# Performance work log

Measured on AMD Instinct MI355X. Metric: run time of the kernel, lower is better.

The kernel has to match this reference:

```python
import jax, jax.numpy as jnp
import numpy as np

N = 100_000   # nodes
D = 128       # emb_size
E = 1_600_000 # edges (avg degree 16)
K = 64        # K1 (channel 0 pooling clusters)
LAYERS = 2


def _l2norm(x):
    # F.normalize(x, dim=-1, p=2) with eps=1e-12
    return x / jnp.maximum(jnp.linalg.norm(x, axis=-1, keepdims=True), 1e-12)


def setup_inputs() -> dict:
    key = jax.random.key(0)
    ks = jax.random.split(key, 9)
    return {
        "adj": jax.random.uniform(ks[0], (N,), dtype=jnp.float32),
        "edge_row": jax.random.randint(ks[1], (E,), 0, N),
        "edge_col": jax.random.randint(ks[2], (E,), 0, N),
        "edge_val": jax.random.uniform(ks[3], (E,), dtype=jnp.float32),
        "embedding": jax.random.normal(ks[4], (N, D), dtype=jnp.float32) * 0.02,
        "W_item0": jax.random.normal(ks[5], (D, D), dtype=jnp.float32) * 0.05,
        "W_item1": jax.random.normal(ks[6], (D, D), dtype=jnp.float32) * 0.05,
        "W_i1": jax.random.normal(ks[7], (D, D), dtype=jnp.float32) * 0.05,
        "W_i2": jax.random.normal(ks[8], (D, K), dtype=jnp.float32) * 0.05,
        "channel": 0,
    }


def reference(adj, edge_row, edge_col, edge_val, embedding,
              W_item0, W_item1, W_i1, W_i2, channel):
    n = adj.shape[0]

    def spmm(x):  # sparse [N,N] @ dense [N,D] via COO gather + segment_sum
        return jax.ops.segment_sum(edge_val[:, None] * x[edge_col], edge_row,
                                   num_segments=n)

    x = embedding
    final = [x]
    finalh = []
    for W in (W_item0, W_item1):  # structurally distinct per-layer weights
        x = spmm(x @ W)                                   # [N,D]
        H1 = jax.nn.relu(x @ W_i1 + x)                    # [N,D]
        H1 = jax.nn.softmax(H1 @ W_i2, axis=1)            # [N,K]
        h = H1.T * adj                                    # [K,N]
        h = h * (1.0 / (jnp.sum(h, axis=0) + 1e-8))       # column-normalize
        h = H1 @ (h @ x)                                  # [N,K]@[K,D] -> [N,D]
        x = h + x
        final.append(_l2norm(x))
        finalh.append(_l2norm(h))
    item_embeddings = sum(final) / (LAYERS + 1)
    hs = sum(finalh) / LAYERS
    return item_embeddings, hs
```

## Files before the change

### kernel.cpp

```cpp
#include <hip/hip_runtime.h>

constexpr int DD = 128;
constexpr int KK = 64;
constexpr int NBLK_C2 = 512;
constexpr int CH = 512;

typedef __attribute__((ext_vector_type(8))) short bf16x8;
typedef __attribute__((ext_vector_type(4))) float f32x4;

union U4 { unsigned u[4]; int4 i4; bf16x8 v; };

__device__ inline unsigned bf16_rne(float x) {
  unsigned u = __float_as_uint(x);
  u += 0x7fff + ((u >> 16) & 1);
  return u >> 16;
}
__device__ inline float bf16f(unsigned h) { return __uint_as_float(h << 16); }
__device__ inline void split2(float a, float b, unsigned& hi, unsigned& lo) {
  const unsigned h0 = bf16_rne(a), h1 = bf16_rne(b);
  const unsigned l0 = bf16_rne(a - bf16f(h0)), l1 = bf16_rne(b - bf16f(h1));
  hi = h0 | (h1 << 16);
  lo = l0 | (l1 << 16);
}

__global__ void k_prepW(const float* __restrict__ W, unsigned* __restrict__ Whi,
                        unsigned* __restrict__ Wlo) {
  const int id = blockIdx.x * 256 + threadIdx.x;
  const int j = id & 3, l = (id >> 2) & 63, t = (id >> 8) & 7, ks = id >> 11;
  const int k0 = 32 * ks + 8 * (l >> 4) + 2 * j;
  const int col = 16 * t + (l & 15);
  const float e0 = W[k0 * 128 + col], e1 = W[(k0 + 1) * 128 + col];
  unsigned hi, lo;
  split2(e0, e1, hi, lo);
  Whi[id] = hi;
  Wlo[id] = lo;
}

__global__ void k_prepWs(const float* __restrict__ W, unsigned* __restrict__ Wf) {
  const int id = blockIdx.x * 256 + threadIdx.x;
  const int j = id & 3, l = (id >> 2) & 63, t = (id >> 8) & 3, ks = id >> 10;
  const int k0 = 32 * ks + 8 * (l >> 4) + 2 * j;
  const int col = 16 * t + (l & 15);
  const unsigned h0 = bf16_rne(W[k0 * 64 + col]);
  const unsigned h1 = bf16_rne(W[(k0 + 1) * 64 + col]);
  Wf[id] = h0 | (h1 << 16);
}

__global__ void k_prepM(const float* __restrict__ M, unsigned* __restrict__ Mhi,
                        unsigned* __restrict__ Mlo) {
  const int id = blockIdx.x * 256 + threadIdx.x;
  const int j = id & 3, l = (id >> 2) & 63, t = (id >> 8) & 7, ks = id >> 11;
  const int k0 = 32 * ks + 8 * (l >> 4) + 2 * j;
  const int col = 16 * t + (l & 15);
  unsigned hi, lo;
  split2(M[k0 * 128 + col], M[(k0 + 1) * 128 + col], hi, lo);
  Mhi[id] = hi;
  Mlo[id] = lo;
}

__global__ __launch_bounds__(512) void k_gemm_mfma(const float* __restrict__ X,
                                                   const unsigned* __restrict__ Whi,
                                                   const unsigned* __restrict__ Wlo,
                                                   unsigned short* __restrict__ Yb,
                                                   int n) {
  __shared__ unsigned sb[2 * 8192];
  {
    const int t = threadIdx.x;
    uint4* d0 = (uint4*)sb;
    const uint4* s0 = (const uint4*)Whi;
#pragma unroll
    for (int i = 0; i < 4; ++i) d0[t + 512 * i] = s0[t + 512 * i];
    uint4* d1 = (uint4*)(sb + 8192);
    const uint4* s1 = (const uint4*)Wlo;
#pragma unroll
    for (int i = 0; i < 4; ++i) d1[t + 512 * i] = s1[t + 512 * i];
  }
  __syncthreads();
  const int wave = threadIdx.x >> 6, lane = threadIdx.x & 63;
  const int l15 = lane & 15, lhi = lane >> 4;
  const int row0 = blockIdx.x * 256 + wave * 32;
  if (row0 >= n) return;
  f32x4 acc[2][8];
#pragma unroll
  for (int rt = 0; rt < 2; ++rt)
#pragma unroll
    for (int t = 0; t < 8; ++t) acc[rt][t] = (f32x4){0.f, 0.f, 0.f, 0.f};
#pragma unroll
  for (int ks = 0; ks < 4; ++ks) {
    U4 ah[2], al[2];
#pragma unroll
    for (int rt = 0; rt < 2; ++rt) {
      int r = row0 + rt * 16 + l15;
      if (r >= n) r = n - 1;
      const float4 x0 = *(const float4*)&X[(size_t)r * DD + ks * 32 + lhi * 8];
      const float4 x1 = *(const float4*)&X[(size_t)r * DD + ks * 32 + lhi * 8 + 4];
      split2(x0.x, x0.y, ah[rt].u[0], al[rt].u[0]);
      split2(x0.z, x0.w, ah[rt].u[1], al[rt].u[1]);
      split2(x1.x, x1.y, ah[rt].u[2], al[rt].u[2]);
      split2(x1.z, x1.w, ah[rt].u[3], al[rt].u[3]);
    }
#pragma unroll
    for (int t = 0; t < 8; ++t) {
      U4 bh, bl;
      const int off = ((ks * 8 + t) * 64 + lane) * 4;
      bh.i4 = *(const int4*)&sb[off];
      bl.i4 = *(const int4*)&sb[8192 + off];
#pragma unroll
      for (int rt = 0; rt < 2; ++rt) {
        acc[rt][t] = __builtin_amdgcn_mfma_f32_16x16x32_bf16(ah[rt].v, bh.v, acc[rt][t], 0, 0, 0);
        acc[rt][t] = __builtin_amdgcn_mfma_f32_16x16x32_bf16(al[rt].v, bh.v, acc[rt][t], 0, 0, 0);
        acc[rt][t] = __builtin_amdgcn_mfma_f32_16x16x32_bf16(ah[rt].v, bl.v, acc[rt][t], 0, 0, 0);
      }
    }
  }
#pragma unroll
  for (int rt = 0; rt < 2; ++rt)
#pragma unroll
    for (int rr = 0; rr < 4; ++rr) {
      const int row = row0 + rt * 16 + lhi * 4 + rr;
      if (row < n) {
#pragma unroll
        for (int t = 0; t < 8; ++t)
          Yb[(size_t)row * DD + t * 16 + l15] =
              (unsigned short)bf16_rne(acc[rt][t][rr]);
      }
    }
}

__global__ void k_hist(const int* __restrict__ er, int* __restrict__ cnt, int E) {
  for (long e = (long)blockIdx.x * blockDim.x + threadIdx.x; e < E;
       e += (long)gridDim.x * blockDim.x)
    atomicAdd(&cnt[er[e]], 1);
}

__global__ __launch_bounds__(256) void k_chunksum(const int* __restrict__ cnt,
                                                  int* __restrict__ csum, int n) {
  const int c = blockIdx.x, t = threadIdx.x;
  const int i0 = c * CH + 2 * t;
  int s2 = 0;
  if (i0 < n) s2 += cnt[i0];
  if (i0 + 1 < n) s2 += cnt[i0 + 1];
#pragma unroll
  for (int off = 32; off >= 1; off >>= 1) s2 += __shfl_xor(s2, off);
  __shared__ int ws_[4];
  if ((t & 63) == 0) ws_[t >> 6] = s2;
  __syncthreads();
  if (t == 0) csum[c] = ws_[0] + ws_[1] + ws_[2] + ws_[3];
}

__global__ __launch_bounds__(256) void k_chunkscan(const int* __restrict__ csum,
                                                   int* __restrict__ coff, int nch) {
  __shared__ int s[256];
  const int t = threadIdx.x;
  const int v = (t < nch) ? csum[t] : 0;
  s[t] = v;
  __syncthreads();
  for (int off = 1; off < 256; off <<= 1) {
    const int u = (t >= off) ? s[t - off] : 0;
    __syncthreads();
    s[t] += u;
    __syncthreads();
  }
  coff[t] = s[t] - v;
}

__global__ __launch_bounds__(256) void k_rowptr(const int* __restrict__ cnt,
                                                const int* __restrict__ coff,
                                                int* __restrict__ rowptr,
                                                int n, int E) {
  const int c = blockIdx.x, t = threadIdx.x;
  const int i0 = c * CH + 2 * t, i1 = i0 + 1;
  const int v0 = (i0 < n) ? cnt[i0] : 0;
  const int v1 = (i1 < n) ? cnt[i1] : 0;
  __shared__ int s[256];
  const int s2 = v0 + v1;
  s[t] = s2;
  __syncthreads();
  for (int off = 1; off < 256; off <<= 1) {
    const int u = (t >= off) ? s[t - off] : 0;
    __syncthreads();
    s[t] += u;
    __syncthreads();
  }
  const int excl = s[t] - s2 + coff[c];
  if (i0 < n) rowptr[i0] = excl;
  if (i1 < n) rowptr[i1] = excl + v0;
  if (c == 0 && t == 0) rowptr[n] = E;
}

__global__ void k_scatter(const int* __restrict__ er, const int* __restrict__ ec,
                          const float* __restrict__ ev,
                          const int* __restrict__ rowptr, int* __restrict__ cur,
                          int2* __restrict__ erec, int E, int n) {
  const int rng = blockIdx.x & 7;
  const int g = blockIdx.x >> 3;
  const long e_lo = (long)g * E / 256;
  const long e_hi = (long)(g + 1) * E / 256;
  const int r_lo = (int)((long)rng * n / 8);
  const int r_hi = (int)((long)(rng + 1) * n / 8);
  for (long e = e_lo + threadIdx.x; e < e_hi; e += 256) {
    const int r = er[e];
    if (r >= r_lo && r < r_hi) {
      const int pos = rowptr[r] + atomicAdd(&cur[r], 1);
      erec[pos] = make_int2(ec[e], __float_as_int(ev[e]));
    }
  }
}

__global__ __launch_bounds__(256) void k_spmm_csr(const int* __restrict__ rowptr,
                                                  const int2* __restrict__ erec,
                                                  const unsigned* __restrict__ Yb,
                                                  float* __restrict__ Xo, int n) {
  const int lane = threadIdx.x & 63;
  const int c0 = 2 * lane;
  const long gw = (long)blockIdx.x * 4 + (threadIdx.x >> 6);
  const long nw = (long)gridDim.x * 4;
  for (long row = gw; row < n; row += nw) {
    const int b = rowptr[row], e2 = rowptr[row + 1];
    float a0 = 0.f, a1 = 0.f, b0 = 0.f, b1 = 0.f;
    float c00 = 0.f, c1 = 0.f, d0 = 0.f, d1 = 0.f;
    int e = b;
    for (; e + 4 <= e2; e += 4) {
      const int2 r0 = erec[e], r1 = erec[e + 1];
      const int2 r2 = erec[e + 2], r3 = erec[e + 3];
      const unsigned q0 = Yb[(size_t)r0.x * (DD / 2) + lane];
      const unsigned q1 = Yb[(size_t)r1.x * (DD / 2) + lane];
      const unsigned q2 = Yb[(size_t)r2.x * (DD / 2) + lane];
      const unsigned q3 = Yb[(size_t)r3.x * (DD / 2) + lane];
      const float v0 = __int_as_float(r0.y), v1 = __int_as_float(r1.y);
      const float v2 = __int_as_float(r2.y), v3 = __int_as_float(r3.y);
      a0 = fmaf(v0, __uint_as_float(q0 << 16), a0);
      a1 = fmaf(v0, __uint_as_float(q0 & 0xffff0000u), a1);
      b0 = fmaf(v1, __uint_as_float(q1 << 16), b0);
      b1 = fmaf(v1, __uint_as_float(q1 & 0xffff0000u), b1);
      c00 = fmaf(v2, __uint_as_float(q2 << 16), c00);
      c1 = fmaf(v2, __uint_as_float(q2 & 0xffff0000u), c1);
      d0 = fmaf(v3, __uint_as_float(q3 << 16), d0);
      d1 = fmaf(v3, __uint_as_float(q3 & 0xffff0000u), d1);
    }
    for (; e + 2 <= e2; e += 2) {
      const int2 r0 = erec[e], r1 = erec[e + 1];
      const float v0 = __int_as_float(r0.y), v1 = __int_as_float(r1.y);
      const unsigned q0 = Yb[(size_t)r0.x * (DD / 2) + lane];
      const unsigned q1 = Yb[(size_t)r1.x * (DD / 2) + lane];
      a0 = fmaf(v0, __uint_as_float(q0 << 16), a0);
      a1 = fmaf(v0, __uint_as_float(q0 & 0xffff0000u), a1);
      b0 = fmaf(v1, __uint_as_float(q1 << 16), b0);
      b1 = fmaf(v1, __uint_as_float(q1 & 0xffff0000u), b1);
    }
    if (e < e2) {
      const int2 r0 = erec[e];
      const float v = __int_as_float(r0.y);
      const unsigned q = Yb[(size_t)r0.x * (DD / 2) + lane];
      a0 = fmaf(v, __uint_as_float(q << 16), a0);
      a1 = fmaf(v, __uint_as_float(q & 0xffff0000u), a1);
    }
    *(float2*)&Xo[(size_t)row * DD + c0] =
        make_float2((a0 + b0) + (c00 + d0), (a1 + b1) + (c1 + d1));
  }
}

__global__ __launch_bounds__(512) void k_c1_mfma(const float* __restrict__ X,
                                                 const unsigned* __restrict__ W1hi,
                                                 const unsigned* __restrict__ W1lo,
                                                 const unsigned* __restrict__ W2f,
                                                 const float* __restrict__ adj,
                                                 float* __restrict__ H1g,
                                                 float* __restrict__ trow, int n) {
  __shared__ unsigned s1[2 * 8192];
  __shared__ unsigned s2[4096];
  __shared__ unsigned h1s[8 * 16 * 68];
  {
    const int t = threadIdx.x;
    uint4* d0 = (uint4*)s1;
    const uint4* sA = (const uint4*)W1hi;
    const uint4* sB = (const uint4*)W1lo;
#pragma unroll
    for (int i = 0; i < 4; ++i) d0[t + 512 * i] = sA[t + 512 * i];
    uint4* d1 = (uint4*)(s1 + 8192);
#pragma unroll
    for (int i = 0; i < 4; ++i) d1[t + 512 * i] = sB[t + 512 * i];
    uint4* d2 = (uint4*)s2;
    const uint4* sC = (const uint4*)W2f;
#pragma unroll
    for (int i = 0; i < 2; ++i) d2[t + 512 * i] = sC[t + 512 * i];
  }
  __syncthreads();
  const int wave = threadIdx.x >> 6, lane = threadIdx.x & 63;
  const int l15 = lane & 15, lhi = lane >> 4;
  unsigned* __restrict__ h1w = h1s + wave * (16 * 68);
  const int row0 = blockIdx.x * 128 + wave * 16;
  if (row0 >= n) return;

  U4 ah[4], al[4];
#pragma unroll
  for (int ks = 0; ks < 4; ++ks) {
    int r = row0 + l15;
    if (r >= n) r = n - 1;
    const float4 x0 = *(const float4*)&X[(size_t)r * DD + ks * 32 + lhi * 8];
    const float4 x1 = *(const float4*)&X[(size_t)r * DD + ks * 32 + lhi * 8 + 4];
    split2(x0.x, x0.y, ah[ks].u[0], al[ks].u[0]);
    split2(x0.z, x0.w, ah[ks].u[1], al[ks].u[1]);
    split2(x1.x, x1.y, ah[ks].u[2], al[ks].u[2]);
    split2(x1.z, x1.w, ah[ks].u[3], al[ks].u[3]);
  }
  f32x4 acc1[8];
#pragma unroll
  for (int t = 0; t < 8; ++t) acc1[t] = (f32x4){0.f, 0.f, 0.f, 0.f};
#pragma unroll
  for (int ks = 0; ks < 4; ++ks) {
#pragma unroll
    for (int t = 0; t < 8; ++t) {
      U4 bh, bl;
      const int off = ((ks * 8 + t) * 64 + lane) * 4;
      bh.i4 = *(const int4*)&s1[off];
      bl.i4 = *(const int4*)&s1[8192 + off];
      acc1[t] = __builtin_amdgcn_mfma_f32_16x16x32_bf16(ah[ks].v, bh.v, acc1[t], 0, 0, 0);
      acc1[t] = __builtin_amdgcn_mfma_f32_16x16x32_bf16(al[ks].v, bh.v, acc1[t], 0, 0, 0);
      acc1[t] = __builtin_amdgcn_mfma_f32_16x16x32_bf16(ah[ks].v, bl.v, acc1[t], 0, 0, 0);
    }
  }

  unsigned short* __restrict__ h16 = (unsigned short*)h1w;
#pragma unroll
  for (int rr = 0; rr < 4; ++rr) {
    int row = row0 + 4 * lhi + rr;
    if (row >= n) row = n - 1;
    const float* __restrict__ xr = X + (size_t)row * DD;
#pragma unroll
    for (int t = 0; t < 8; ++t) {
      float v = acc1[t][rr] + xr[16 * t + l15];
      v = fmaxf(v, 0.f);
      h16[(4 * lhi + rr) * 136 + 16 * t + l15] = (unsigned short)bf16_rne(v);
    }
  }

  f32x4 acc3[4];
#pragma unroll
  for (int t = 0; t < 4; ++t) acc3[t] = (f32x4){0.f, 0.f, 0.f, 0.f};
#pragma unroll
  for (int ks = 0; ks < 4; ++ks) {
    U4 a3;
    a3.i4 = *(const int4*)&h1w[l15 * 68 + ks * 16 + lhi * 4];
#pragma unroll
    for (int t = 0; t < 4; ++t) {
      U4 b3;
      b3.i4 = *(const int4*)&s2[((ks * 4 + t) * 64 + lane) * 4];
      acc3[t] = __builtin_amdgcn_mfma_f32_16x16x32_bf16(a3.v, b3.v, acc3[t], 0, 0, 0);
    }
  }

#pragma unroll
  for (int rr = 0; rr < 4; ++rr) {
    const int row = row0 + 4 * lhi + rr;
    float z0 = acc3[0][rr], z1 = acc3[1][rr], z2 = acc3[2][rr], z3 = acc3[3][rr];
    float m = fmaxf(fmaxf(z0, z1), fmaxf(z2, z3));
#pragma unroll
    for (int off = 8; off >= 1; off >>= 1) m = fmaxf(m, __shfl_xor(m, off));
    const float p0 = expf(z0 - m), p1 = expf(z1 - m);
    const float p2 = expf(z2 - m), p3 = expf(z3 - m);
    float s = p0 + p1 + p2 + p3;
#pragma unroll
    for (int off = 8; off >= 1; off >>= 1) s += __shfl_xor(s, off);
    const float inv = 1.0f / s;
    if (row < n) {
      float* __restrict__ hr = H1g + (size_t)row * KK;
      hr[l15] = p0 * inv;
      hr[16 + l15] = p1 * inv;
      hr[32 + l15] = p2 * inv;
      hr[48 + l15] = p3 * inv;
      if (l15 == 0) {
        const float a = adj[row];
        trow[row] = a / (a + 1e-8f);
      }
    }
  }
}

__global__ __launch_bounds__(1024, 4) void k_c2(const float* __restrict__ X,
                                                const float* __restrict__ trow,
                                                const float* __restrict__ H1g,
                                                float* __restrict__ Mpart, int n) {
  __shared__ float cmb[3 * 4 * 16 * 2 * 64];
  const int t = threadIdx.x;
  const int wave = t >> 6, lane = t & 63;
  const int rg = wave >> 2, kg = wave & 3;
  const int kb = kg * 16;
  const int d0 = 2 * lane;
  float macc[16][2];
#pragma unroll
  for (int j = 0; j < 16; ++j) { macc[j][0] = 0.f; macc[j][1] = 0.f; }
  const int bx = blockIdx.x;
  for (long row = (long)bx + 512L * rg; row < n; row += 2048L) {
    const int r = __builtin_amdgcn_readfirstlane((int)row);
    const float tr = trow[r];
    const float2 xv = *(const float2*)&X[(size_t)r * DD + d0];
    const float px0 = tr * xv.x, px1 = tr * xv.y;
    const float* __restrict__ hrow = H1g + (size_t)r * KK + kb;
#pragma unroll
    for (int j = 0; j < 16; ++j) {
      const float hj = hrow[j];
      macc[j][0] = fmaf(hj, px0, macc[j][0]);
      macc[j][1] = fmaf(hj, px1, macc[j][1]);
    }
  }
  if (rg > 0) {
    float* __restrict__ dst = cmb + ((rg - 1) * 4 + kg) * (16 * 2 * 64);
#pragma unroll
    for (int j = 0; j < 16; ++j) {
      dst[(2 * j + 0) * 64 + lane] = macc[j][0];
      dst[(2 * j + 1) * 64 + lane] = macc[j][1];
    }
  }
  __syncthreads();
  if (rg == 0) {
#pragma unroll
    for (int g = 0; g < 3; ++g) {
      const float* __restrict__ src = cmb + (g * 4 + kg) * (16 * 2 * 64);
#pragma unroll
      for (int j = 0; j < 16; ++j) {
        macc[j][0] += src[(2 * j + 0) * 64 + lane];
        macc[j][1] += src[(2 * j + 1) * 64 + lane];
      }
    }
    float* __restrict__ mp = Mpart + (size_t)bx * (KK * DD);
#pragma unroll
    for (int j = 0; j < 16; ++j)
      *(float2*)&mp[(kb + j) * DD + d0] = make_float2(macc[j][0], macc[j][1]);
  }
}

__global__ void k_dred1(const float* __restrict__ Mpart, float* __restrict__ Mp2) {
  const int j = blockIdx.x * blockDim.x + threadIdx.x;
  const int i = j & (KK * DD - 1);
  const int c = j >> 13;
  float s = 0.f;
#pragma unroll
  for (int q = 0; q < 16; ++q)
    s += Mpart[(size_t)(c * 16 + q) * (KK * DD) + i];
  Mp2[(size_t)c * (KK * DD) + i] = s;
}

__global__ void k_dred2(const float* __restrict__ Mp2, float* __restrict__ Mg) {
  const int i = blockIdx.x * blockDim.x + threadIdx.x;
  float s = 0.f;
#pragma unroll
  for (int c = 0; c < 32; ++c) s += Mp2[(size_t)c * (KK * DD) + i];
  Mg[i] = s;
}

__global__ __launch_bounds__(512) void k_fin_mfma(const float* __restrict__ H1g,
                                                  const unsigned* __restrict__ Mhi,
                                                  const unsigned* __restrict__ Mlo,
                                                  const float* __restrict__ emb,
                                                  float* __restrict__ Xb,
                                                  float* __restrict__ out,
                                                  int n, int first) {
  __shared__ unsigned sm[2 * 4096];
  {
    const int t = threadIdx.x;
    uint4* d0 = (uint4*)sm;
    const uint4* s0 = (const uint4*)Mhi;
#pragma unroll
    for (int i = 0; i < 2; ++i) d0[t + 512 * i] = s0[t + 512 * i];
    uint4* d1 = (uint4*)(sm + 4096);
    const uint4* s1 = (const uint4*)Mlo;
#pragma unroll
    for (int i = 0; i < 2; ++i) d1[t + 512 * i] = s1[t + 512 * i];
  }
  __syncthreads();
  const int wave = threadIdx.x >> 6, lane = threadIdx.x & 63;
  const int l15 = lane & 15, lhi = lane >> 4;
  const size_t hoff = (size_t)n * DD;
  const int row0 = blockIdx.x * 128 + wave * 16;
  if (row0 >= n) return;

  U4 ah[2], al[2];
  {
    int ra = row0 + l15;
    if (ra >= n) ra = n - 1;
    const float* __restrict__ hp = H1g + (size_t)ra * KK;
#pragma unroll
    for (int ks = 0; ks < 2; ++ks) {
      const float4 x0 = *(const float4*)&hp[ks * 32 + lhi * 8];
      const float4 x1 = *(const float4*)&hp[ks * 32 + lhi * 8 + 4];
      split2(x0.x, x0.y, ah[ks].u[0], al[ks].u[0]);
      split2(x0.z, x0.w, ah[ks].u[1], al[ks].u[1]);
      split2(x1.x, x1.y, ah[ks].u[2], al[ks].u[2]);
      split2(x1.z, x1.w, ah[ks].u[3], al[ks].u[3]);
    }
  }
  f32x4 acc[8];
#pragma unroll
  for (int t = 0; t < 8; ++t) acc[t] = (f32x4){0.f, 0.f, 0.f, 0.f};
#pragma unroll
  for (int ks = 0; ks < 2; ++ks) {
#pragma unroll
    for (int t = 0; t < 8; ++t) {
      U4 bh, bl;
      const int off = ((ks * 8 + t) * 64 + lane) * 4;
      bh.i4 = *(const int4*)&sm[off];
      bl.i4 = *(const int4*)&sm[4096 + off];
      acc[t] = __builtin_amdgcn_mfma_f32_16x16x32_bf16(ah[ks].v, bh.v, acc[t], 0, 0, 0);
      acc[t] = __builtin_amdgcn_mfma_f32_16x16x32_bf16(al[ks].v, bh.v, acc[t], 0, 0, 0);
      acc[t] = __builtin_amdgcn_mfma_f32_16x16x32_bf16(ah[ks].v, bl.v, acc[t], 0, 0, 0);
    }
  }
#pragma unroll
  for (int rr = 0; rr < 4; ++rr) {
    const int row = row0 + 4 * lhi + rr;
    const int rc = (row < n) ? row : (n - 1);
    float hh[8], xx[8];
    float sh = 0.f, sx = 0.f;
#pragma unroll
    for (int t = 0; t < 8; ++t) {
      const float xv = Xb[(size_t)rc * DD + 16 * t + l15];
      hh[t] = acc[t][rr];
      xx[t] = hh[t] + xv;
      sh = fmaf(hh[t], hh[t], sh);
      sx = fmaf(xx[t], xx[t], sx);
    }
#pragma unroll
    for (int off = 8; off >= 1; off >>= 1) {
      sh += __shfl_xor(sh, off);
      sx += __shfl_xor(sx, off);
    }
    const float ih = 0.5f / fmaxf(sqrtf(sh), 1e-12f);
    const float ix = (1.0f / 3.0f) / fmaxf(sqrtf(sx), 1e-12f);
    if (row < n) {
#pragma unroll
      for (int t = 0; t < 8; ++t) {
        const size_t oi = (size_t)row * DD + 16 * t + l15;
        Xb[oi] = xx[t];
        float ci, ch;
        if (first) {
          ci = emb[oi] * (1.0f / 3.0f);
          ch = 0.f;
        } else {
          ci = out[oi];
          ch = out[hoff + oi];
        }
        out[oi] = ci + xx[t] * ix;
        out[hoff + oi] = ch + hh[t] * ih;
      }
    }
  }
}

extern "C" void kernel_launch(void* const* d_in, const int* in_sizes, int n_in,
                              void* d_out, int out_size, void* d_ws, size_t ws_size,
                              hipStream_t stream) {
  const float* adj  = (const float*)d_in[0];
  const int*   erow = (const int*)d_in[1];
  const int*   ecol = (const int*)d_in[2];
  const float* eval = (const float*)d_in[3];
  const float* emb  = (const float*)d_in[4];
  const float* W0   = (const float*)d_in[5];
  const float* W1   = (const float*)d_in[6];
  const float* Wi1  = (const float*)d_in[7];
  const float* Wi2  = (const float*)d_in[8];
  const int n = in_sizes[0];
  const int E = in_sizes[1];
  float* out = (float*)d_out;

  float* xb    = (float*)d_ws;
  float* yb    = xb + (size_t)n * DD;
  unsigned short* Ybf = (unsigned short*)yb;
  float* H1g   = yb + (size_t)n * (DD / 2);
  float* Mpart = H1g + (size_t)n * KK;
  float* Mp2   = Mpart + (size_t)NBLK_C2 * KK * DD;
  float* Mg    = Mp2 + (size_t)32 * KK * DD;
  int*   cnt    = (int*)(Mg + KK * DD);
  int*   rowptr = cnt + n;
  int*   csum   = rowptr + n + 4;
  int*   coff   = csum + 256;
  int2*  erec   = (int2*)(coff + 256);
  float* trow   = (float*)(erec + E);
  unsigned* w0hi  = (unsigned*)(trow + n);
  unsigned* w0lo  = w0hi + 8192;
  unsigned* w1hi_ = w0lo + 8192;
  unsigned* w1lo_ = w1hi_ + 8192;
  unsigned* wi1hi = w1lo_ + 8192;
  unsigned* wi1lo = wi1hi + 8192;
  unsigned* wi2f  = wi1lo + 8192;
  unsigned* mhi   = wi2f + 4096;
  unsigned* mlo   = mhi + 4096;

  const int NCH = (n + CH - 1) / CH;

  k_prepW<<<32, 256, 0, stream>>>(W0, w0hi, w0lo);
  k_prepW<<<32, 256, 0, stream>>>(W1, w1hi_, w1lo_);
  k_prepW<<<32, 256, 0, stream>>>(Wi1, wi1hi, wi1lo);
  k_prepWs<<<16, 256, 0, stream>>>(Wi2, wi2f);

  hipMemsetAsync(cnt, 0, (size_t)n * sizeof(int), stream);
  k_hist<<<2048, 256, 0, stream>>>(erow, cnt, E);
  k_chunksum<<<NCH, 256, 0, stream>>>(cnt, csum, n);
  k_chunkscan<<<1, 256, 0, stream>>>(csum, coff, NCH);
  k_rowptr<<<NCH, 256, 0, stream>>>(cnt, coff, rowptr, n, E);
  hipMemsetAsync(cnt, 0, (size_t)n * sizeof(int), stream);
  k_scatter<<<2048, 256, 0, stream>>>(erow, ecol, eval, rowptr, cnt, erec, E, n);

  const int g_gm  = (n + 255) / 256;
  const int g_c1m = (n + 127) / 128;
  const int g_fin = (n + 127) / 128;

  for (int L = 0; L < 2; ++L) {
    const unsigned* Whi = (L == 0) ? w0hi : w1hi_;
    const unsigned* Wlo = (L == 0) ? w0lo : w1lo_;
    const float* Xin = (L == 0) ? emb : xb;
    k_gemm_mfma<<<g_gm, 512, 0, stream>>>(Xin, Whi, Wlo, Ybf, n);
    k_spmm_csr<<<2048, 256, 0, stream>>>(rowptr, erec, (const unsigned*)Ybf, xb, n);
    k_c1_mfma<<<g_c1m, 512, 0, stream>>>(xb, wi1hi, wi1lo, wi2f, adj, H1g, trow, n);
    k_c2<<<NBLK_C2, 1024, 0, stream>>>(xb, trow, H1g, Mpart, n);
    k_dred1<<<1024, 256, 0, stream>>>(Mpart, Mp2);
    k_dred2<<<32, 256, 0, stream>>>(Mp2, Mg);
    k_prepM<<<16, 256, 0, stream>>>(Mg, mhi, mlo);
    k_fin_mfma<<<g_fin, 512, 0, stream>>>(H1g, mhi, mlo, emb, xb, out, n, (L == 0) ? 1 : 0);
  }
}
```

Before: 711.0 us.

## Read low weight halves from global, simplify CSR scatter, widen SpMM unroll

The GEMM and c1 kernels stop staging the low bf16 weight halves (and W2) in shared memory and read them straight from global/L2, which halves LDS use and may raise occupancy at the cost of more global loads inside the MFMA loop. The edge scatter drops its 8-way row-range partitioning, so each edge is read once instead of eight times. Atomics are now spread across the whole row range, which changes locality. The SpMM gather loop is unrolled to 8 independent edges with 8 accumulator pairs to expose more memory-level parallelism.

```diff
diff --git a/kernel.cpp b/kernel.cpp
--- a/kernel.cpp
+++ b/kernel.cpp
@@ -63,17 +63,13 @@
                                                    const unsigned* __restrict__ Wlo,
                                                    unsigned short* __restrict__ Yb,
                                                    int n) {
-  __shared__ unsigned sb[2 * 8192];
+  __shared__ unsigned sb[8192];
   {
     const int t = threadIdx.x;
     uint4* d0 = (uint4*)sb;
     const uint4* s0 = (const uint4*)Whi;
 #pragma unroll
     for (int i = 0; i < 4; ++i) d0[t + 512 * i] = s0[t + 512 * i];
-    uint4* d1 = (uint4*)(sb + 8192);
-    const uint4* s1 = (const uint4*)Wlo;
-#pragma unroll
-    for (int i = 0; i < 4; ++i) d1[t + 512 * i] = s1[t + 512 * i];
   }
   __syncthreads();
   const int wave = threadIdx.x >> 6, lane = threadIdx.x & 63;
@@ -104,7 +100,7 @@
       U4 bh, bl;
       const int off = ((ks * 8 + t) * 64 + lane) * 4;
       bh.i4 = *(const int4*)&sb[off];
-      bl.i4 = *(const int4*)&sb[8192 + off];
+      bl.i4 = *(const int4*)&Wlo[off];
 #pragma unroll
       for (int rt = 0; rt < 2; ++rt) {
         acc[rt][t] = __builtin_amdgcn_mfma_f32_16x16x32_bf16(ah[rt].v, bh.v, acc[rt][t], 0, 0, 0);
@@ -191,19 +187,12 @@
 __global__ void k_scatter(const int* __restrict__ er, const int* __restrict__ ec,
                           const float* __restrict__ ev,
                           const int* __restrict__ rowptr, int* __restrict__ cur,
-                          int2* __restrict__ erec, int E, int n) {
-  const int rng = blockIdx.x & 7;
-  const int g = blockIdx.x >> 3;
-  const long e_lo = (long)g * E / 256;
-  const long e_hi = (long)(g + 1) * E / 256;
-  const int r_lo = (int)((long)rng * n / 8);
-  const int r_hi = (int)((long)(rng + 1) * n / 8);
-  for (long e = e_lo + threadIdx.x; e < e_hi; e += 256) {
+                          int2* __restrict__ erec, int E) {
+  for (long e = (long)blockIdx.x * blockDim.x + threadIdx.x; e < E;
+       e += (long)gridDim.x * blockDim.x) {
     const int r = er[e];
-    if (r >= r_lo && r < r_hi) {
-      const int pos = rowptr[r] + atomicAdd(&cur[r], 1);
-      erec[pos] = make_int2(ec[e], __float_as_int(ev[e]));
-    }
+    const int pos = rowptr[r] + atomicAdd(&cur[r], 1);
+    erec[pos] = make_int2(ec[e], __float_as_int(ev[e]));
   }
 }
 
@@ -217,46 +206,44 @@
   const long nw = (long)gridDim.x * 4;
   for (long row = gw; row < n; row += nw) {
     const int b = rowptr[row], e2 = rowptr[row + 1];
-    float a0 = 0.f, a1 = 0.f, b0 = 0.f, b1 = 0.f;
-    float c00 = 0.f, c1 = 0.f, d0 = 0.f, d1 = 0.f;
+    float a0[8], a1[8];
+#pragma unroll
+    for (int i = 0; i < 8; ++i) { a0[i] = 0.f; a1[i] = 0.f; }
     int e = b;
-    for (; e + 4 <= e2; e += 4) {
+    for (; e + 8 <= e2; e += 8) {
+      int2 rr[8];
+      unsigned qq[8];
+#pragma unroll
+      for (int i = 0; i < 8; ++i) rr[i] = erec[e + i];
+#pragma unroll
+      for (int i = 0; i < 8; ++i) qq[i] = Yb[(size_t)rr[i].x * (DD / 2) + lane];
+#pragma unroll
+      for (int i = 0; i < 8; ++i) {
+        const float v = __int_as_float(rr[i].y);
+        a0[i] = fmaf(v, __uint_as_float(qq[i] << 16), a0[i]);
+        a1[i] = fmaf(v, __uint_as_float(qq[i] & 0xffff0000u), a1[i]);
+      }
+    }
+    for (; e + 2 <= e2; e += 2) {
       const int2 r0 = erec[e], r1 = erec[e + 1];
-      const int2 r2 = erec[e + 2], r3 = erec[e + 3];
       const unsigned q0 = Yb[(size_t)r0.x * (DD / 2) + lane];
       const unsigned q1 = Yb[(size_t)r1.x * (DD / 2) + lane];
-      const unsigned q2 = Yb[(size_t)r2.x * (DD / 2) + lane];
-      const unsigned q3 = Yb[(size_t)r3.x * (DD / 2) + lane];
       const float v0 = __int_as_float(r0.y), v1 = __int_as_float(r1.y);
-      const float v2 = __int_as_float(r2.y), v3 = __int_as_float(r3.y);
-      a0 = fmaf(v0, __uint_as_float(q0 << 16), a0);
-      a1 = fmaf(v0, __uint_as_float(q0 & 0xffff0000u), a1);
-      b0 = fmaf(v1, __uint_as_float(q1 << 16), b0);
-      b1 = fmaf(v1, __uint_as_float(q1 & 0xffff0000u), b1);
-      c00 = fmaf(v2, __uint_as_float(q2 << 16), c00);
-      c1 = fmaf(v2, __uint_as_float(q2 & 0xffff0000u), c1);
-      d0 = fmaf(v3, __uint_as_float(q3 << 16), d0);
-      d1 = fmaf(v3, __uint_as_float(q3 & 0xffff0000u), d1);
-    }
-    for (; e + 2 <= e2; e += 2) {
-      const int2 r0 = erec[e], r1 = erec[e + 1];
-      const float v0 = __int_as_float(r0.y), v1 = __int_as_float(r1.y);
-      const unsigned q0 = Yb[(size_t)r0.x * (DD / 2) + lane];
-      const unsigned q1 = Yb[(size_t)r1.x * (DD / 2) + lane];
-      a0 = fmaf(v0, __uint_as_float(q0 << 16), a0);
-      a1 = fmaf(v0, __uint_as_float(q0 & 0xffff0000u), a1);
-      b0 = fmaf(v1, __uint_as_float(q1 << 16), b0);
-      b1 = fmaf(v1, __uint_as_float(q1 & 0xffff0000u), b1);
+      a0[0] = fmaf(v0, __uint_as_float(q0 << 16), a0[0]);
+      a1[0] = fmaf(v0, __uint_as_float(q0 & 0xffff0000u), a1[0]);
+      a0[1] = fmaf(v1, __uint_as_float(q1 << 16), a0[1]);
+      a1[1] = fmaf(v1, __uint_as_float(q1 & 0xffff0000u), a1[1]);
     }
     if (e < e2) {
       const int2 r0 = erec[e];
       const float v = __int_as_float(r0.y);
       const unsigned q = Yb[(size_t)r0.x * (DD / 2) + lane];
-      a0 = fmaf(v, __uint_as_float(q << 16), a0);
-      a1 = fmaf(v, __uint_as_float(q & 0xffff0000u), a1);
-    }
-    *(float2*)&Xo[(size_t)row * DD + c0] =
-        make_float2((a0 + b0) + (c00 + d0), (a1 + b1) + (c1 + d1));
+      a0[0] = fmaf(v, __uint_as_float(q << 16), a0[0]);
+      a1[0] = fmaf(v, __uint_as_float(q & 0xffff0000u), a1[0]);
+    }
+    const float s0 = ((a0[0] + a0[1]) + (a0[2] + a0[3])) + ((a0[4] + a0[5]) + (a0[6] + a0[7]));
+    const float s1 = ((a1[0] + a1[1]) + (a1[2] + a1[3])) + ((a1[4] + a1[5]) + (a1[6] + a1[7]));
+    *(float2*)&Xo[(size_t)row * DD + c0] = make_float2(s0, s1);
   }
 }
 
@@ -267,23 +254,14 @@
                                                  const float* __restrict__ adj,
                                                  float* __restrict__ H1g,
                                                  float* __restrict__ trow, int n) {
-  __shared__ unsigned s1[2 * 8192];
-  __shared__ unsigned s2[4096];
+  __shared__ unsigned s1[8192];
   __shared__ unsigned h1s[8 * 16 * 68];
   {
     const int t = threadIdx.x;
     uint4* d0 = (uint4*)s1;
     const uint4* sA = (const uint4*)W1hi;
-    const uint4* sB = (const uint4*)W1lo;
 #pragma unroll
     for (int i = 0; i < 4; ++i) d0[t + 512 * i] = sA[t + 512 * i];
-    uint4* d1 = (uint4*)(s1 + 8192);
-#pragma unroll
-    for (int i = 0; i < 4; ++i) d1[t + 512 * i] = sB[t + 512 * i];
-    uint4* d2 = (uint4*)s2;
-    const uint4* sC = (const uint4*)W2f;
-#pragma unroll
-    for (int i = 0; i < 2; ++i) d2[t + 512 * i] = sC[t + 512 * i];
   }
   __syncthreads();
   const int wave = threadIdx.x >> 6, lane = threadIdx.x & 63;
@@ -314,7 +292,7 @@
       U4 bh, bl;
       const int off = ((ks * 8 + t) * 64 + lane) * 4;
       bh.i4 = *(const int4*)&s1[off];
-      bl.i4 = *(const int4*)&s1[8192 + off];
+      bl.i4 = *(const int4*)&W1lo[off];
       acc1[t] = __builtin_amdgcn_mfma_f32_16x16x32_bf16(ah[ks].v, bh.v, acc1[t], 0, 0, 0);
       acc1[t] = __builtin_amdgcn_mfma_f32_16x16x32_bf16(al[ks].v, bh.v, acc1[t], 0, 0, 0);
       acc1[t] = __builtin_amdgcn_mfma_f32_16x16x32_bf16(ah[ks].v, bl.v, acc1[t], 0, 0, 0);
@@ -345,7 +323,7 @@
 #pragma unroll
     for (int t = 0; t < 4; ++t) {
       U4 b3;
-      b3.i4 = *(const int4*)&s2[((ks * 4 + t) * 64 + lane) * 4];
+      b3.i4 = *(const int4*)&W2f[((ks * 4 + t) * 64 + lane) * 4];
       acc3[t] = __builtin_amdgcn_mfma_f32_16x16x32_bf16(a3.v, b3.v, acc3[t], 0, 0, 0);
     }
   }
@@ -599,7 +577,7 @@
   k_chunkscan<<<1, 256, 0, stream>>>(csum, coff, NCH);
   k_rowptr<<<NCH, 256, 0, stream>>>(cnt, coff, rowptr, n, E);
   hipMemsetAsync(cnt, 0, (size_t)n * sizeof(int), stream);
-  k_scatter<<<2048, 256, 0, stream>>>(erow, ecol, eval, rowptr, cnt, erec, E, n);
+  k_scatter<<<2048, 256, 0, stream>>>(erow, ecol, eval, rowptr, cnt, erec, E);
 
   const int g_gm  = (n + 255) / 256;
   const int g_c1m = (n + 127) / 128;
```

New measurement: 743.6 us. 4.6% more time.
